# Kernel optimization log

Measured on AMD Instinct MI355X. Metric: run time of the kernel, lower is better.

Reference implementation:

```python
import jax, jax.numpy as jnp
import numpy as np

N_LAYER = 2
DEPTH = 2
D_IN = 64
H1 = 64
N = 8192  # sequence length; H2 == N is required by F * chord_mask


def make_chord(n):
    # eye(n) plus, for k in {0,1}, mask[i, (i + 2^k - 1) % n] = 1
    # k=0 re-sets the diagonal; k=1 sets the (wrapped) superdiagonal.
    eye = jnp.eye(n, dtype=jnp.float32)
    superdiag = jnp.roll(eye, 1, axis=1)  # [i, (i+1)%n] = 1
    return jnp.minimum(eye + superdiag, 1.0)


def setup_inputs() -> dict:
    key = jax.random.key(0)
    ks = jax.random.split(key, 8)
    s_in = 1.0 / np.sqrt(D_IN)
    X = jax.random.normal(ks[0], (N, D_IN), dtype=jnp.float32)
    # g stack: DEPTH x Linear(D_IN -> H1) (requires H1 == D_IN to stack)
    g_w = jax.random.uniform(ks[1], (DEPTH, H1, D_IN), jnp.float32, -s_in, s_in)
    g_b = jax.random.uniform(ks[2], (DEPTH, H1), jnp.float32, -s_in, s_in)
    # f stacks, one per layer m: (DEPTH-1) x Linear(D_IN->D_IN), then Linear(D_IN->H2=N)
    f0_w = jax.random.uniform(ks[3], (N_LAYER, D_IN, D_IN), jnp.float32, -s_in, s_in)
    f0_b = jax.random.uniform(ks[4], (N_LAYER, D_IN), jnp.float32, -s_in, s_in)
    fL_w = jax.random.uniform(ks[5], (N_LAYER, N, D_IN), jnp.float32, -s_in, s_in)
    fL_b = jax.random.uniform(ks[6], (N_LAYER, N), jnp.float32, -s_in, s_in)
    return {"X": X, "g_w": g_w, "g_b": g_b, "f0_w": f0_w, "f0_b": f0_b,
            "fL_w": fL_w, "fL_b": fL_b}


def reference(X, g_w, g_b, f0_w, f0_b, fL_w, fL_b):
    chord_mask = make_chord(N)  # [N, N], ~2 nonzeros per row
    # V0 = g stack applied to X
    V = X
    for d in range(DEPTH):
        V = jax.nn.relu(V @ g_w[d].T + g_b[d])  # [N, H1]
    # chained masked-score matmuls
    for m in range(N_LAYER):
        F = jax.nn.relu(X @ f0_w[m].T + f0_b[m])   # [N, D_IN]
        F = jax.nn.relu(F @ fL_w[m].T + fL_b[m])   # [N, N] dense score
        W = F * chord_mask                          # chord-sparse
        V = W @ V                                   # [N, H1]
    return V
```

## Files before the change

### kernel.cpp

```cpp
#include <hip/hip_runtime.h>


#define NROWS 8192
#define BROWS 16
#define RPW 5

__device__ __forceinline__ float rl(float v, int lane) {
  return __int_as_float(__builtin_amdgcn_readlane(__float_as_int(v), lane));
}

__device__ __forceinline__ float wave_sum(float x) {
  x += __int_as_float(__builtin_amdgcn_update_dpp(0, __float_as_int(x), 0x121, 0xF, 0xF, false));
  x += __int_as_float(__builtin_amdgcn_update_dpp(0, __float_as_int(x), 0x122, 0xF, 0xF, false));
  x += __int_as_float(__builtin_amdgcn_update_dpp(0, __float_as_int(x), 0x124, 0xF, 0xF, false));
  x += __int_as_float(__builtin_amdgcn_update_dpp(0, __float_as_int(x), 0x128, 0xF, 0xF, false));
  float a0 = rl(x, 0), a1 = rl(x, 16), a2 = rl(x, 32), a3 = rl(x, 48);
  return (a0 + a1) + (a2 + a3);
}

__device__ __forceinline__ void stageW(float4 (*Wq)[65], const float* __restrict__ W, int tid) {
  const float4* ws = (const float4*)W;
#pragma unroll
  for (int p = 0; p < 4; ++p) {
    int idx = p * 256 + tid;
    Wq[idx & 15][idx >> 4] = ws[idx];
  }
}

template <int R>
__device__ __forceinline__ void mm64(const float4 (*Wq)[65], int lane,
                                     const float* src, float bias, float* acc) {
#pragma unroll
  for (int r = 0; r < R; ++r) acc[r] = bias;
#pragma unroll 4
  for (int kb = 0; kb < 16; ++kb) {
    float4 w4 = Wq[kb][lane];
#pragma unroll
    for (int r = 0; r < R; ++r) {
      acc[r] = fmaf(rl(src[r], 4 * kb + 0), w4.x, acc[r]);
      acc[r] = fmaf(rl(src[r], 4 * kb + 1), w4.y, acc[r]);
      acc[r] = fmaf(rl(src[r], 4 * kb + 2), w4.z, acc[r]);
      acc[r] = fmaf(rl(src[r], 4 * kb + 3), w4.w, acc[r]);
    }
  }
#pragma unroll
  for (int r = 0; r < R; ++r) acc[r] = fmaxf(acc[r], 0.0f);
}

__global__ __launch_bounds__(256, 2) void fused_smfnet(
    const float* __restrict__ X, const float* __restrict__ g_w,
    const float* __restrict__ g_b, const float* __restrict__ f0_w,
    const float* __restrict__ f0_b, const float* __restrict__ fL_w,
    const float* __restrict__ fL_b, float* __restrict__ out)
{
  __shared__ float4 Wq[16][65];
  __shared__ float V0s[20][65];
  __shared__ float V1s[19][65];

  const int tid  = threadIdx.x;
  const int lane = tid & 63;
  const int wv   = tid >> 6;
  const int r0   = blockIdx.x * BROWS;

  stageW(Wq, g_w, tid);
  float hb  = g_b[lane];
  float vb  = g_b[64 + lane];

  float xr[RPW];
  int grow[RPW];
#pragma unroll
  for (int r = 0; r < RPW; ++r) {
    int L = wv * RPW + r;
    grow[r] = (r0 + L) & (NROWS - 1);
    xr[r] = X[grow[r] * 64 + lane];
  }
  __syncthreads();

  float h[RPW];
  mm64<RPW>(Wq, lane, xr, hb, h);

  __syncthreads();
  stageW(Wq, g_w + 4096, tid);
  __syncthreads();

  float v0[RPW];
  mm64<RPW>(Wq, lane, h, vb, v0);
#pragma unroll
  for (int r = 0; r < RPW; ++r) V0s[wv * RPW + r][lane] = v0[r];

  __syncthreads();
  stageW(Wq, f0_w, tid);
  __syncthreads();

  float tb0 = f0_b[lane];
  float t[RPW];
  mm64<RPW>(Wq, lane, xr, tb0, t);

  float v1[RPW];
#pragma unroll
  for (int r = 0; r < RPW; ++r) {
    int L = wv * RPW + r;
    if (L <= 18) {
      int g   = grow[r];
      int gp1 = (g + 1) & (NROWS - 1);
      float pa = wave_sum(t[r] * fL_w[g * 64 + lane]);
      float pb = wave_sum(t[r] * fL_w[gp1 * 64 + lane]);
      float a  = fmaxf(pa + fL_b[g], 0.0f);
      float b  = fmaxf(pb + fL_b[gp1], 0.0f);
      v1[r] = a * v0[r] + b * V0s[L + 1][lane];
      V1s[L][lane] = v1[r];
    }
  }

  __syncthreads();
  stageW(Wq, f0_w + 4096, tid);
  __syncthreads();

  float tb1 = f0_b[64 + lane];
  mm64<RPW>(Wq, lane, xr, tb1, t);

  const float* fw1 = fL_w + NROWS * 64;
  const float* fb1 = fL_b + NROWS;
#pragma unroll
  for (int r = 0; r < RPW; ++r) {
    int L = wv * RPW + r;
    if (L <= 15) {
      int g   = grow[r];
      int gp1 = (g + 1) & (NROWS - 1);
      float pa = wave_sum(t[r] * fw1[g * 64 + lane]);
      float pb = wave_sum(t[r] * fw1[gp1 * 64 + lane]);
      float a  = fmaxf(pa + fb1[g], 0.0f);
      float b  = fmaxf(pb + fb1[gp1], 0.0f);
      out[g * 64 + lane] = a * v1[r] + b * V1s[L + 1][lane];
    }
  }
}

extern "C" void kernel_launch(void* const* d_in, const int* in_sizes, int n_in,
                              void* d_out, int out_size, void* d_ws, size_t ws_size,
                              hipStream_t stream) {
  const float* X    = (const float*)d_in[0];
  const float* g_w  = (const float*)d_in[1];
  const float* g_b  = (const float*)d_in[2];
  const float* f0_w = (const float*)d_in[3];
  const float* f0_b = (const float*)d_in[4];
  const float* fL_w = (const float*)d_in[5];
  const float* fL_b = (const float*)d_in[6];
  float* out = (float*)d_out;

  fused_smfnet<<<dim3(NROWS / BROWS), dim3(256), 0, stream>>>(
      X, g_w, g_b, f0_w, f0_b, fL_w, fL_b, out);
}
```

Measured before the change: 87.62 us.

## Double-stage weight pairs in LDS and read X rows as uniform scalar loads

Weights are now staged two matrices at a time into a doubled LDS buffer, which removes two of the stage/sync rounds between layers. For the X-consuming matmuls the input row is read directly as wave-uniform float4 loads at a readfirstlane row index, replacing per-lane loads followed by readlane broadcasts. The first layer's halo now covers 17 rows instead of 19, since the second layer only needs one extra row. In exchange, LDS use per block grows, which may reduce occupancy, and X is re-read from memory three times instead of being held in registers.

```diff
diff --git a/kernel.cpp b/kernel.cpp
--- a/kernel.cpp
+++ b/kernel.cpp
@@ -18,18 +18,42 @@
   return (a0 + a1) + (a2 + a3);
 }
 
-__device__ __forceinline__ void stageW(float4 (*Wq)[65], const float* __restrict__ W, int tid) {
+__device__ __forceinline__ void stageW2(float4 (*Wq)[16][65],
+                                        const float* __restrict__ W, int tid) {
   const float4* ws = (const float4*)W;
 #pragma unroll
-  for (int p = 0; p < 4; ++p) {
+  for (int p = 0; p < 8; ++p) {
     int idx = p * 256 + tid;
-    Wq[idx & 15][idx >> 4] = ws[idx];
+    int rem = idx & 1023;
+    Wq[idx >> 10][rem & 15][rem >> 4] = ws[idx];
   }
 }
 
 template <int R>
-__device__ __forceinline__ void mm64(const float4 (*Wq)[65], int lane,
-                                     const float* src, float bias, float* acc) {
+__device__ __forceinline__ void mm64_s(const float4 (*Wq)[65], int lane,
+                                       const float* __restrict__ X,
+                                       const int* growu, float bias, float* acc) {
+#pragma unroll
+  for (int r = 0; r < R; ++r) acc[r] = bias;
+#pragma unroll 4
+  for (int kb = 0; kb < 16; ++kb) {
+    float4 w4 = Wq[kb][lane];
+#pragma unroll
+    for (int r = 0; r < R; ++r) {
+      float4 xq = *(const float4*)(X + (growu[r] << 6) + (kb << 2));
+      acc[r] = fmaf(xq.x, w4.x, acc[r]);
+      acc[r] = fmaf(xq.y, w4.y, acc[r]);
+      acc[r] = fmaf(xq.z, w4.z, acc[r]);
+      acc[r] = fmaf(xq.w, w4.w, acc[r]);
+    }
+  }
+#pragma unroll
+  for (int r = 0; r < R; ++r) acc[r] = fmaxf(acc[r], 0.0f);
+}
+
+template <int R>
+__device__ __forceinline__ void mm64_rl(const float4 (*Wq)[65], int lane,
+                                        const float* src, float bias, float* acc) {
 #pragma unroll
   for (int r = 0; r < R; ++r) acc[r] = bias;
 #pragma unroll 4
@@ -53,55 +77,49 @@
     const float* __restrict__ f0_b, const float* __restrict__ fL_w,
     const float* __restrict__ fL_b, float* __restrict__ out)
 {
-  __shared__ float4 Wq[16][65];
+  __shared__ float4 Wq[2][16][65];
   __shared__ float V0s[20][65];
-  __shared__ float V1s[19][65];
+  __shared__ float V1s[17][65];
 
   const int tid  = threadIdx.x;
   const int lane = tid & 63;
   const int wv   = tid >> 6;
   const int r0   = blockIdx.x * BROWS;
 
-  stageW(Wq, g_w, tid);
+  stageW2(Wq, g_w, tid);
   float hb  = g_b[lane];
   float vb  = g_b[64 + lane];
 
-  float xr[RPW];
-  int grow[RPW];
+  int growu[RPW];
 #pragma unroll
   for (int r = 0; r < RPW; ++r) {
     int L = wv * RPW + r;
-    grow[r] = (r0 + L) & (NROWS - 1);
-    xr[r] = X[grow[r] * 64 + lane];
+    growu[r] = __builtin_amdgcn_readfirstlane((r0 + L) & (NROWS - 1));
   }
   __syncthreads();
 
   float h[RPW];
-  mm64<RPW>(Wq, lane, xr, hb, h);
-
-  __syncthreads();
-  stageW(Wq, g_w + 4096, tid);
-  __syncthreads();
+  mm64_s<RPW>(Wq[0], lane, X, growu, hb, h);
 
   float v0[RPW];
-  mm64<RPW>(Wq, lane, h, vb, v0);
+  mm64_rl<RPW>(Wq[1], lane, h, vb, v0);
 #pragma unroll
   for (int r = 0; r < RPW; ++r) V0s[wv * RPW + r][lane] = v0[r];
 
   __syncthreads();
-  stageW(Wq, f0_w, tid);
+  stageW2(Wq, f0_w, tid);
   __syncthreads();
 
   float tb0 = f0_b[lane];
   float t[RPW];
-  mm64<RPW>(Wq, lane, xr, tb0, t);
+  mm64_s<RPW>(Wq[0], lane, X, growu, tb0, t);
 
   float v1[RPW];
 #pragma unroll
   for (int r = 0; r < RPW; ++r) {
     int L = wv * RPW + r;
-    if (L <= 18) {
-      int g   = grow[r];
+    if (L <= 16) {
+      int g   = growu[r];
       int gp1 = (g + 1) & (NROWS - 1);
       float pa = wave_sum(t[r] * fL_w[g * 64 + lane]);
       float pb = wave_sum(t[r] * fL_w[gp1 * 64 + lane]);
@@ -113,11 +131,8 @@
   }
 
   __syncthreads();
-  stageW(Wq, f0_w + 4096, tid);
-  __syncthreads();
-
   float tb1 = f0_b[64 + lane];
-  mm64<RPW>(Wq, lane, xr, tb1, t);
+  mm64_s<RPW>(Wq[1], lane, X, growu, tb1, t);
 
   const float* fw1 = fL_w + NROWS * 64;
   const float* fb1 = fL_b + NROWS;
@@ -125,7 +140,7 @@
   for (int r = 0; r < RPW; ++r) {
     int L = wv * RPW + r;
     if (L <= 15) {
-      int g   = grow[r];
+      int g   = growu[r];
       int gp1 = (g + 1) & (NROWS - 1);
       float pa = wave_sum(t[r] * fw1[g * 64 + lane]);
       float pb = wave_sum(t[r] * fw1[gp1 * 64 + lane]);
```

Result: faster. 85.11 us (-2.9%).
